# Optimization experiments

Hardware: AMD Instinct MI355X
Metric: run time of the kernel (lower is better)

## Reference

```python
import jax, jax.numpy as jnp
import numpy as np

M = 16
C = 7 * M          # 112, stage-8 channels
CLS = 20
TOPK = 3
NQ = 20000         # current-frame active sites at stage 8
NS = 8192          # support-frame active sites at stage 8
SCALE = 128.0      # voxel coordinate range at this depth


def setup_inputs() -> dict:
    key = jax.random.key(0)
    ks = jax.random.split(key, 9)
    coords_q = jax.random.uniform(ks[0], (NQ, 3), jnp.float32) * SCALE
    coords_s = jax.random.uniform(ks[1], (NS, 3), jnp.float32) * SCALE
    x7 = jax.random.normal(ks[2], (NQ, C), jnp.float32)
    feat_s7 = jax.random.normal(ks[3], (NS, C), jnp.float32)
    feat_s = jax.random.normal(ks[4], (NS, C), jnp.float32)
    w_attn = jax.random.normal(ks[5], (C,), jnp.float32) * 0.1
    W1 = jax.random.normal(ks[6], (2 * C, C), jnp.float32) * (1.0 / np.sqrt(2 * C))
    gamma = jnp.ones((C,), jnp.float32)
    beta = jnp.zeros((C,), jnp.float32)
    W2 = jax.random.normal(ks[7], (C, C), jnp.float32) * (1.0 / np.sqrt(C))
    W_cls = jax.random.normal(ks[8], (C, CLS), jnp.float32) * (1.0 / np.sqrt(C))
    b_cls = jnp.zeros((CLS,), jnp.float32)
    return dict(coords_q=coords_q, coords_s=coords_s, x7=x7, feat_s7=feat_s7,
                feat_s=feat_s, w_attn=w_attn, W1=W1, gamma=gamma, beta=beta,
                W2=W2, W_cls=W_cls, b_cls=b_cls)


def reference(coords_q, coords_s, x7, feat_s7, feat_s, w_attn, W1, gamma, beta, W2, W_cls, b_cls):
    # GlobalMeanAttentionPooling: attention-weighted mean over support sites -> global vector [C]
    a = jax.nn.softmax(feat_s7 @ w_attn)          # [NS]
    g = a @ feat_s7                                # [C]
    # GlobalMaskLayer: channel-wise sigmoid gating of current-frame features
    feat_q = x7 * jax.nn.sigmoid(g)                # [NQ, C]
    # DistMatchLayer_v4: top-3 nearest support voxels per query, softmax(-d2) weighting
    q2 = jnp.sum(coords_q * coords_q, -1, keepdims=True)   # [NQ, 1]
    s2 = jnp.sum(coords_s * coords_s, -1)                  # [NS]
    d2 = q2 + s2[None, :] - 2.0 * (coords_q @ coords_s.T)  # [NQ, NS]
    negd, idx = jax.lax.top_k(-d2, TOPK)                   # [NQ, K]
    w = jax.nn.softmax(negd, axis=-1)                      # [NQ, K]
    matched = jnp.einsum('nk,nkc->nc', w, feat_s[idx])     # [NQ, C]
    # tune_sub: 1x1 subconv (14m->7m) -> BN(eval affine) + ReLU -> 1x1 subconv (7m->7m)
    h = jnp.concatenate([feat_q, matched], -1) @ W1        # [NQ, C]
    h = jax.nn.relu(h * gamma + beta) @ W2                 # [NQ, C]
    # final classifier linear
    return h @ W_cls + b_cls                               # [NQ, CLS]
```

## Files before the change

kernel.cpp:

```cpp
#include <hip/hip_runtime.h>

#define NQv 20000
#define NSv 8192
#define Cv  112
#define CLSv 20
#define INFF 3.4e38f
#define JINF 0x7fffffff

#define GC 16
#define NCELL 4096
#define CELLH 8.0f
#define INVH 0.125f

#define POOLB 32
#define PT 1024
#define PNW (POOLB * PT / 64)

#define MQ 16
#define MB (NQv / MQ)
#define MT 256
#define WS_START 3616
#define WS_PTS4  5668
#define WS_W1TH  38440
#define WS_W1TL  50984
#define WS_W2TH  63528
#define WS_W2TL  70696
#define WS_WCT   77864
#define WS_GATE  80104

typedef __attribute__((ext_vector_type(8))) short bf16x8;
typedef __attribute__((ext_vector_type(4))) float f32x4;
typedef unsigned short us;
typedef unsigned long long u64;

__device__ __forceinline__ float bf2f(us u) {
    union { unsigned int i; float f; } v; v.i = ((unsigned int)u) << 16; return v.f;
}
__device__ __forceinline__ us f2bf(float f) {
    union { float f; unsigned int i; } v; v.f = f;
    unsigned int r = v.i + 0x7fffu + ((v.i >> 16) & 1u);
    return (us)(r >> 16);
}
__device__ __forceinline__ void split(float v, us& h, us& l) {
    h = f2bf(v); l = f2bf(v - bf2f(h));
}

__device__ __forceinline__ u64 mkkey(float e, int j) {
    union { float f; unsigned int i; } v; v.f = e;
    unsigned int ue = v.i ^ ((unsigned int)((int)v.i >> 31) | 0x80000000u);
    return ((u64)ue << 32) | (unsigned int)j;
}
__device__ __forceinline__ float keyval(u64 k) {
    unsigned int ue = (unsigned int)(k >> 32);
    unsigned int u = ue ^ ((unsigned int)((int)(~ue) >> 31) | 0x80000000u);
    union { unsigned int i; float f; } v; v.i = u; return v.f;
}
__device__ __forceinline__ u64 umin64(u64 a, u64 b) { return a < b ? a : b; }
__device__ __forceinline__ u64 umax64(u64 a, u64 b) { return a > b ? a : b; }

__global__ __launch_bounds__(PT) void k_prep(const float* __restrict__ cs,
                                             const float* __restrict__ fs7,
                                             const float* __restrict__ wat,
                                             const float* __restrict__ W1,
                                             const float* __restrict__ W2,
                                             const float* __restrict__ Wc,
                                             float* __restrict__ ws) {
    int b = blockIdx.x, tid = threadIdx.x;

    if (b == POOLB + 1) {
        us* w1h = (us*)(ws + WS_W1TH);
        us* w1l = (us*)(ws + WS_W1TL);
        for (int idx = tid; idx < Cv * 224; idx += PT) {
            int c = idx / 224, k = idx - c * 224;
            us h, l; split(W1[k * Cv + c], h, l);
            w1h[c * 224 + k] = h; w1l[c * 224 + k] = l;
        }
        return;
    }
    if (b == POOLB + 2) {
        us* w2h = (us*)(ws + WS_W2TH);
        us* w2l = (us*)(ws + WS_W2TL);
        for (int idx = tid; idx < Cv * 128; idx += PT) {
            int c = idx >> 7, k = idx & 127;
            float v = (k < Cv) ? W2[k * Cv + c] : 0.f;
            us h, l; split(v, h, l);
            w2h[c * 128 + k] = h; w2l[c * 128 + k] = l;
        }
        float* wct = ws + WS_WCT;
        for (int idx = tid; idx < CLSv * Cv; idx += PT) {
            int cls = idx / Cv, k = idx - cls * Cv;
            wct[cls * Cv + k] = Wc[k * CLSv + cls];
        }
        return;
    }
    if (b == POOLB) {
        __shared__ int cnt[NCELL];
        __shared__ int wsum[PT / 64];
        us* startg = (us*)(ws + WS_START);
        float4* pts4 = (float4*)(ws + WS_PTS4);
        int lane = tid & 63, wv = tid >> 6;
        for (int i = tid; i < NCELL; i += PT) cnt[i] = 0;
        __syncthreads();
        float xx[8], yy[8], zz[8]; int cid[8]; int pp[8];
        #pragma unroll
        for (int k = 0; k < NSv / PT; ++k) {
            int p = k * PT + tid;
            pp[k] = p;
            xx[k] = cs[3 * p]; yy[k] = cs[3 * p + 1]; zz[k] = cs[3 * p + 2];
            int cx = (int)(xx[k] * INVH), cy = (int)(yy[k] * INVH), cz = (int)(zz[k] * INVH);
            cx = cx > 15 ? 15 : cx; cy = cy > 15 ? 15 : cy; cz = cz > 15 ? 15 : cz;
            cid[k] = (cz * GC + cy) * GC + cx;
            atomicAdd(&cnt[cid[k]], 1);
        }
        __syncthreads();
        int base = tid * 4;
        int c0 = cnt[base], c1 = cnt[base + 1], c2 = cnt[base + 2], c3 = cnt[base + 3];
        int local = c0 + c1 + c2 + c3;
        int inc = local;
        #pragma unroll
        for (int off = 1; off < 64; off <<= 1) {
            int v = __shfl_up(inc, off, 64);
            if (lane >= off) inc += v;
        }
        if (lane == 63) wsum[wv] = inc;
        __syncthreads();
        if (tid < PT / 64) {
            int v = wsum[tid];
            #pragma unroll
            for (int off = 1; off < 16; off <<= 1) {
                int o = __shfl_up(v, off, 64);
                if (tid >= off) v += o;
            }
            wsum[tid] = v;
        }
        __syncthreads();
        int wbase = (wv == 0) ? 0 : wsum[wv - 1];
        int run = wbase + inc - local;
        startg[base] = (us)run;     cnt[base] = run;     run += c0;
        startg[base + 1] = (us)run; cnt[base + 1] = run; run += c1;
        startg[base + 2] = (us)run; cnt[base + 2] = run; run += c2;
        startg[base + 3] = (us)run; cnt[base + 3] = run;
        if (tid == 0) startg[NCELL] = (us)NSv;
        __syncthreads();
        #pragma unroll
        for (int k = 0; k < NSv / PT; ++k) {
            int slot = atomicAdd(&cnt[cid[k]], 1);
            pts4[slot] = make_float4(-2.f * xx[k], -2.f * yy[k], -2.f * zz[k], (float)pp[k]);
        }
        return;
    }

    __shared__ float red[PT / 64][Cv + 1];
    int gtid = b * PT + tid;
    int wid = gtid >> 6, lw = tid >> 6, lane = gtid & 63, l2 = lane * 2;
    float2 wa = make_float2(0.f, 0.f);
    if (lane < 56) wa = *(const float2*)(wat + l2);
    float gx = 0.f, gy = 0.f, z = 0.f;
    for (int g = 0; g < 2; ++g) {
        float2 f[8]; float part[8];
        #pragma unroll
        for (int u = 0; u < 8; ++u) {
            int i = wid + (g * 8 + u) * PNW;
            f[u] = (lane < 56) ? *(const float2*)(fs7 + i * Cv + l2) : make_float2(0.f, 0.f);
            part[u] = f[u].x * wa.x + f[u].y * wa.y;
        }
        #pragma unroll
        for (int off = 32; off; off >>= 1)
            #pragma unroll
            for (int u = 0; u < 8; ++u) part[u] += __shfl_xor(part[u], off, 64);
        #pragma unroll
        for (int u = 0; u < 8; ++u) {
            float p = __expf(part[u]);
            gx = fmaf(p, f[u].x, gx); gy = fmaf(p, f[u].y, gy); z += p;
        }
    }
    if (lane < 56) { red[lw][l2] = gx; red[lw][l2 + 1] = gy; }
    if (lane == 0) red[lw][Cv] = z;
    __syncthreads();
    if (tid < Cv + 1) {
        float s = 0.f;
        #pragma unroll
        for (int i = 0; i < PT / 64; ++i) s += red[i][tid];
        ws[tid * POOLB + b] = s;
    }
}

__global__ __launch_bounds__(128) void k_gate(float* __restrict__ ws) {
    int tid = threadIdx.x;
    if (tid < Cv) {
        float st = 0.f, zt = 0.f;
        const float* pr = ws + tid * POOLB;
        const float* zr = ws + Cv * POOLB;
        #pragma unroll
        for (int b = 0; b < POOLB; ++b) { st += pr[b]; zt += zr[b]; }
        ws[WS_GATE + tid] = 1.0f / (1.0f + __expf(-(st / zt)));
    }
}

__device__ __forceinline__ void scan_run(const float4* __restrict__ pts4,
                                         int a, int b, float qx, float qy, float qz,
                                         float& E0, float& E1, float& E2,
                                         int& J0, int& J1, int& J2) {
    for (int k = a; k < b; ++k) {
        float4 P = pts4[k];
        float x = -0.5f * P.x, y = -0.5f * P.y, z = -0.5f * P.z;
        float s2 = fmaf(x, x, fmaf(y, y, z * z));
        float e = fmaf(qx, P.x, fmaf(qy, P.y, fmaf(qz, P.z, s2)));
        int j = (int)P.w;
        bool lt2 = (e < E2) || (e == E2 && j < J2);
        if (lt2) {
            bool lt1 = (e < E1) || (e == E1 && j < J1);
            bool lt0 = (e < E0) || (e == E0 && j < J0);
            E2 = lt1 ? E1 : e;              J2 = lt1 ? J1 : j;
            E1 = lt0 ? E0 : (lt1 ? e : E1); J1 = lt0 ? J0 : (lt1 ? j : J1);
            if (lt0) { E0 = e; J0 = j; }
        }
    }
}

__global__ __launch_bounds__(MT, 6) void k_fused(
        const float* __restrict__ cq,
        const float* __restrict__ x7, const float* __restrict__ fs,
        const float* __restrict__ gma, const float* __restrict__ bta,
        const float* __restrict__ bc, const float* __restrict__ ws,
        float* __restrict__ out) {
    __shared__ __align__(16) us vb[2 * MQ * 232];
    __shared__ __align__(16) us hbh[MQ * 136];
    __shared__ __align__(16) us hbl[MQ * 136];

    us* vbh = vb;
    us* vbl = vb + MQ * 232;
    float* h2f = (float*)vb;

    const us* __restrict__ startg = (const us*)(ws + WS_START);
    const float4* __restrict__ pts4 = (const float4*)(ws + WS_PTS4);

    int tid = threadIdx.x;
    int q0 = blockIdx.x * MQ;
    int sub = tid & 15;
    int qq  = tid >> 4;
    int q   = q0 + qq;

    float4 px[4], g4[4];
    if (sub < 7) {
        const float4* xr = (const float4*)(x7 + q * Cv + sub * 16);
        px[0] = xr[0]; px[1] = xr[1]; px[2] = xr[2]; px[3] = xr[3];
        const float4* gr = (const float4*)(ws + WS_GATE + sub * 16);
        g4[0] = gr[0]; g4[1] = gr[1]; g4[2] = gr[2]; g4[3] = gr[3];
    }
    {
        int zq = tid >> 4, kk = Cv + (tid & 15);
        hbh[zq * 136 + kk] = 0; hbl[zq * 136 + kk] = 0;
    }

    u64 K0 = ~0ull, K1 = ~0ull, K2 = ~0ull;
    {
        float qx = cq[3 * q], qy = cq[3 * q + 1], qz = cq[3 * q + 2];
        float q2 = fmaf(qx, qx, fmaf(qy, qy, qz * qz));
        int cx = (int)(qx * INVH), cy = (int)(qy * INVH), cz = (int)(qz * INVH);
        cx = cx > 15 ? 15 : cx; cy = cy > 15 ? 15 : cy; cz = cz > 15 ? 15 : cz;
        float E0 = INFF, E1 = INFF, E2 = INFF;
        int   J0 = JINF, J1 = JINF, J2 = JINF;

        #pragma unroll
        for (int c = sub; c < 27; c += 16) {
            int dz = c / 9 - 1, dy = (c / 3) % 3 - 1, dx = c % 3 - 1;
            int xc = cx + dx, yc = cy + dy, zc = cz + dz;
            if ((unsigned)xc < 16u && (unsigned)yc < 16u && (unsigned)zc < 16u) {
                int ccell = (zc * GC + yc) * GC + xc;
                scan_run(pts4, startg[ccell], startg[ccell + 1], qx, qy, qz,
                         E0, E1, E2, J0, J1, J2);
            }
        }

        bool done = false;
        for (int s = 2; ; ++s) {
            if (!done) {
                K0 = mkkey(E0, J0); K1 = mkkey(E1, J1); K2 = mkkey(E2, J2);
                #pragma unroll
                for (int off = 1; off < 16; off <<= 1) {
                    u64 b0 = __shfl_xor(K0, off, 64);
                    u64 b1 = __shfl_xor(K1, off, 64);
                    u64 b2 = __shfl_xor(K2, off, 64);
                    u64 xx = umax64(K0, b0), yy = umin64(K1, b1);
                    u64 zz = umax64(K1, b1), uu = umin64(K2, b2);
                    K0 = umin64(K0, b0);
                    u64 n1 = umin64(xx, yy);
                    K2 = umin64(umin64(umax64(xx, yy), zz), uu);
                    K1 = n1;
                }
            }
            if (s > 15) break;
            if (!done) {
                int r = s - 1;
                int xl = cx - r > 0 ? cx - r : 0, xh = cx + r < 15 ? cx + r : 15;
                int yl = cy - r > 0 ? cy - r : 0, yh = cy + r < 15 ? cy + r : 15;
                int zl = cz - r > 0 ? cz - r : 0, zh = cz + r < 15 ? cz + r : 15;
                float fx = INFF, fy = INFF, fz = INFF;
                if (xl > 0)  fx = qx - xl * CELLH;
                if (xh < 15) fx = fminf(fx, (xh + 1) * CELLH - qx);
                if (yl > 0)  fy = qy - yl * CELLH;
                if (yh < 15) fy = fminf(fy, (yh + 1) * CELLH - qy);
                if (zl > 0)  fz = qz - zl * CELLH;
                if (zh < 15) fz = fminf(fz, (zh + 1) * CELLH - qz);
                float dmin = fminf(fx, fminf(fy, fz));
                float t2 = keyval(K2);
                if (dmin * dmin > t2 + q2 + 0.5f) {
                    done = true;
                } else if (s == 2) {
                    for (int idx = sub; idx < 125; idx += 16) {
                        int dz = idx / 25 - 2;
                        int rem = idx - (dz + 2) * 25;
                        int dy = rem / 5 - 2;
                        int dx = rem - (dy + 2) * 5 - 2;
                        int ax = dx < 0 ? -dx : dx, ay = dy < 0 ? -dy : dy, az = dz < 0 ? -dz : dz;
                        if (ax != 2 && ay != 2 && az != 2) continue;
                        int xc = cx + dx, yc = cy + dy, zc = cz + dz;
                        if ((unsigned)xc > 15u || (unsigned)yc > 15u || (unsigned)zc > 15u) continue;
                        int ccell = (zc * GC + yc) * GC + xc;
                        scan_run(pts4, startg[ccell], startg[ccell + 1], qx, qy, qz,
                                 E0, E1, E2, J0, J1, J2);
                    }
                } else {
                    int side = 2 * s + 1, s2n = side * side, tot = s2n * side;
                    for (int idx = sub; idx < tot; idx += 16) {
                        int dz = idx / s2n - s;
                        int rem = idx - (dz + s) * s2n;
                        int dy = rem / side - s;
                        int dx = rem - (dy + s) * side - s;
                        int ax = dx < 0 ? -dx : dx, ay = dy < 0 ? -dy : dy, az = dz < 0 ? -dz : dz;
                        if (ax != s && ay != s && az != s) continue;
                        int xc = cx + dx, yc = cy + dy, zc = cz + dz;
                        if ((unsigned)xc > 15u || (unsigned)yc > 15u || (unsigned)zc > 15u) continue;
                        int ccell = (zc * GC + yc) * GC + xc;
                        scan_run(pts4, startg[ccell], startg[ccell + 1], qx, qy, qz,
                                 E0, E1, E2, J0, J1, J2);
                    }
                }
            }
            if (__all(done)) break;
        }
    }

    {
        unsigned int A0 = (unsigned int)K0;
        unsigned int A1 = (unsigned int)K1;
        unsigned int A2 = (unsigned int)K2;
        if (A0 >= NSv) A0 = 0;
        if (A1 >= NSv) A1 = 0;
        if (A2 >= NSv) A2 = 0;
        if (sub < 7) {
            int k0 = sub * 16;
            float vals[16];
            #pragma unroll
            for (int i = 0; i < 4; ++i) {
                float4 v = px[i], g = g4[i];
                vals[i * 4]     = v.x * g.x;
                vals[i * 4 + 1] = v.y * g.y;
                vals[i * 4 + 2] = v.z * g.z;
                vals[i * 4 + 3] = v.w * g.w;
            }
            #pragma unroll
            for (int i = 0; i < 16; ++i) {
                us h, l; split(vals[i], h, l);
                vbh[qq * 232 + k0 + i] = h;
                vbl[qq * 232 + k0 + i] = l;
            }
        } else if (sub < 14) {
            float e0 = keyval(K0), e1 = keyval(K1), e2 = keyval(K2);
            float w1v = __expf(e0 - e1);
            float w2v = __expf(e0 - e2);
            float iw  = 1.0f / (1.0f + w1v + w2v);
            float w0 = iw, w1 = w1v * iw, w2 = w2v * iw;
            int kk = (sub - 7) * 16;
            const float4* r0 = (const float4*)(fs + A0 * Cv + kk);
            const float4* r1 = (const float4*)(fs + A1 * Cv + kk);
            const float4* r2 = (const float4*)(fs + A2 * Cv + kk);
            float vals[16];
            #pragma unroll
            for (int i = 0; i < 4; ++i) {
                float4 a = r0[i], b = r1[i], c = r2[i];
                vals[i * 4]     = w0 * a.x + w1 * b.x + w2 * c.x;
                vals[i * 4 + 1] = w0 * a.y + w1 * b.y + w2 * c.y;
                vals[i * 4 + 2] = w0 * a.z + w1 * b.z + w2 * c.z;
                vals[i * 4 + 3] = w0 * a.w + w1 * b.w + w2 * c.w;
            }
            int k0 = Cv + kk;
            #pragma unroll
            for (int i = 0; i < 16; ++i) {
                us h, l; split(vals[i], h, l);
                vbh[qq * 232 + k0 + i] = h;
                vbl[qq * 232 + k0 + i] = l;
            }
        }
    }
    __syncthreads();

    int w = tid >> 6, lane = tid & 63, quad = lane >> 4, l16 = lane & 15;
    bool two = (w < 3);
    int cc0 = w * 16 + l16;
    int cc1 = two ? (w + 4) * 16 + l16 : cc0;

    {
        f32x4 acc0 = {0.f, 0.f, 0.f, 0.f};
        f32x4 acc1 = {0.f, 0.f, 0.f, 0.f};
        const us* w1h0 = (const us*)(ws + WS_W1TH) + cc0 * 224;
        const us* w1l0 = (const us*)(ws + WS_W1TL) + cc0 * 224;
        const us* w1h1 = (const us*)(ws + WS_W1TH) + cc1 * 224;
        const us* w1l1 = (const us*)(ws + WS_W1TL) + cc1 * 224;
        #pragma unroll
        for (int ks = 0; ks < 7; ++ks) {
            int ko = ks * 32 + quad * 8;
            bf16x8 ah = *(const bf16x8*)(vbh + l16 * 232 + ko);
            bf16x8 al = *(const bf16x8*)(vbl + l16 * 232 + ko);
            bf16x8 bh0 = *(const bf16x8*)(w1h0 + ko);
            bf16x8 bl0 = *(const bf16x8*)(w1l0 + ko);
            acc0 = __builtin_amdgcn_mfma_f32_16x16x32_bf16(ah, bh0, acc0, 0, 0, 0);
            acc0 = __builtin_amdgcn_mfma_f32_16x16x32_bf16(al, bh0, acc0, 0, 0, 0);
            acc0 = __builtin_amdgcn_mfma_f32_16x16x32_bf16(ah, bl0, acc0, 0, 0, 0);
            if (two) {
                bf16x8 bh1 = *(const bf16x8*)(w1h1 + ko);
                bf16x8 bl1 = *(const bf16x8*)(w1l1 + ko);
                acc1 = __builtin_amdgcn_mfma_f32_16x16x32_bf16(ah, bh1, acc1, 0, 0, 0);
                acc1 = __builtin_amdgcn_mfma_f32_16x16x32_bf16(al, bh1, acc1, 0, 0, 0);
                acc1 = __builtin_amdgcn_mfma_f32_16x16x32_bf16(ah, bl1, acc1, 0, 0, 0);
            }
        }
        float g0 = gma[cc0], b0 = bta[cc0];
        float g1 = two ? gma[cc1] : 0.f, b1 = two ? bta[cc1] : 0.f;
        #pragma unroll
        for (int r = 0; r < 4; ++r) {
            int dq = quad * 4 + r;
            float h = fmaf(acc0[r], g0, b0); h = h > 0.f ? h : 0.f;
            us hh, ll; split(h, hh, ll);
            hbh[dq * 136 + cc0] = hh; hbl[dq * 136 + cc0] = ll;
            if (two) {
                float h2 = fmaf(acc1[r], g1, b1); h2 = h2 > 0.f ? h2 : 0.f;
                split(h2, hh, ll);
                hbh[dq * 136 + cc1] = hh; hbl[dq * 136 + cc1] = ll;
            }
        }
    }
    __syncthreads();

    {
        f32x4 acc0 = {0.f, 0.f, 0.f, 0.f};
        f32x4 acc1 = {0.f, 0.f, 0.f, 0.f};
        const us* w2h0 = (const us*)(ws + WS_W2TH) + cc0 * 128;
        const us* w2l0 = (const us*)(ws + WS_W2TL) + cc0 * 128;
        const us* w2h1 = (const us*)(ws + WS_W2TH) + cc1 * 128;
        const us* w2l1 = (const us*)(ws + WS_W2TL) + cc1 * 128;
        #pragma unroll
        for (int ks = 0; ks < 4; ++ks) {
            int ko = ks * 32 + quad * 8;
            bf16x8 ah = *(const bf16x8*)(hbh + l16 * 136 + ko);
            bf16x8 al = *(const bf16x8*)(hbl + l16 * 136 + ko);
            bf16x8 bh0 = *(const bf16x8*)(w2h0 + ko);
            bf16x8 bl0 = *(const bf16x8*)(w2l0 + ko);
            acc0 = __builtin_amdgcn_mfma_f32_16x16x32_bf16(ah, bh0, acc0, 0, 0, 0);
            acc0 = __builtin_amdgcn_mfma_f32_16x16x32_bf16(al, bh0, acc0, 0, 0, 0);
            acc0 = __builtin_amdgcn_mfma_f32_16x16x32_bf16(ah, bl0, acc0, 0, 0, 0);
            if (two) {
                bf16x8 bh1 = *(const bf16x8*)(w2h1 + ko);
                bf16x8 bl1 = *(const bf16x8*)(w2l1 + ko);
                acc1 = __builtin_amdgcn_mfma_f32_16x16x32_bf16(ah, bh1, acc1, 0, 0, 0);
                acc1 = __builtin_amdgcn_mfma_f32_16x16x32_bf16(al, bh1, acc1, 0, 0, 0);
                acc1 = __builtin_amdgcn_mfma_f32_16x16x32_bf16(ah, bl1, acc1, 0, 0, 0);
            }
        }
        #pragma unroll
        for (int r = 0; r < 4; ++r) {
            int dq = quad * 4 + r;
            h2f[dq * 116 + cc0] = acc0[r];
            if (two) h2f[dq * 116 + cc1] = acc1[r];
        }
    }
    __syncthreads();

    for (int it = tid; it < MQ * CLSv; it += MT) {
        int cls = it % CLSv, oq = it / CLSv;
        const float4* wr = (const float4*)(ws + WS_WCT + cls * Cv);
        const float4* hr = (const float4*)(h2f + oq * 116);
        float a = bc[cls];
        #pragma unroll 7
        for (int i = 0; i < 28; ++i) {
            float4 h = hr[i], v = wr[i];
            a = fmaf(h.x, v.x, fmaf(h.y, v.y, fmaf(h.z, v.z, fmaf(h.w, v.w, a))));
        }
        out[(q0 + oq) * CLSv + cls] = a;
    }
}

extern "C" void kernel_launch(void* const* d_in, const int* in_sizes, int n_in,
                              void* d_out, int out_size, void* d_ws, size_t ws_size,
                              hipStream_t stream) {
    const float* cq  = (const float*)d_in[0];
    const float* cs  = (const float*)d_in[1];
    const float* x7  = (const float*)d_in[2];
    const float* fs7 = (const float*)d_in[3];
    const float* fs  = (const float*)d_in[4];
    const float* wat = (const float*)d_in[5];
    const float* W1  = (const float*)d_in[6];
    const float* gma = (const float*)d_in[7];
    const float* bta = (const float*)d_in[8];
    const float* W2  = (const float*)d_in[9];
    const float* Wc  = (const float*)d_in[10];
    const float* bc  = (const float*)d_in[11];
    float* ws  = (float*)d_ws;
    float* out = (float*)d_out;

    k_prep<<<POOLB + 3, PT, 0, stream>>>(cs, fs7, wat, W1, W2, Wc, ws);
    k_gate<<<1, 128, 0, stream>>>(ws);
    k_fused<<<MB, MT, 0, stream>>>(cq, x7, fs, gma, bta, bc, ws, out);
}
```

Measured before the change: 149.8 us.

## Double query tile, fold gate kernel into fused kernel, unroll neighbor scan

Raises the per-block query tile from 16 to 32 with 512 threads, so each of 7 waves owns one 16-column output slice and reuses its weight fragments across two query row-tiles. This is meant to halve the weight loads per query in the MFMA stages. The separate gate kernel launch is removed and every block now recomputes the sigmoid gate into shared memory, which saves a launch but adds a redundant reduction per block. The grid scan loop is unrolled by two to overlap point loads, and one of the eight waves sits idle during the matmul stages.

```diff
diff --git a/kernel.cpp b/kernel.cpp
--- a/kernel.cpp
+++ b/kernel.cpp
@@ -16,9 +16,9 @@
 #define PT 1024
 #define PNW (POOLB * PT / 64)
 
-#define MQ 16
+#define MQ 32
 #define MB (NQv / MQ)
-#define MT 256
+#define MT 512
 #define WS_START 3616
 #define WS_PTS4  5668
 #define WS_W1TH  38440
@@ -26,7 +26,6 @@
 #define WS_W2TH  63528
 #define WS_W2TL  70696
 #define WS_WCT   77864
-#define WS_GATE  80104
 
 typedef __attribute__((ext_vector_type(8))) short bf16x8;
 typedef __attribute__((ext_vector_type(4))) float f32x4;
@@ -185,15 +184,20 @@
     }
 }
 
-__global__ __launch_bounds__(128) void k_gate(float* __restrict__ ws) {
-    int tid = threadIdx.x;
-    if (tid < Cv) {
-        float st = 0.f, zt = 0.f;
-        const float* pr = ws + tid * POOLB;
-        const float* zr = ws + Cv * POOLB;
-        #pragma unroll
-        for (int b = 0; b < POOLB; ++b) { st += pr[b]; zt += zr[b]; }
-        ws[WS_GATE + tid] = 1.0f / (1.0f + __expf(-(st / zt)));
+__device__ __forceinline__ void ins_pt(float4 P, float qx, float qy, float qz,
+                                       float& E0, float& E1, float& E2,
+                                       int& J0, int& J1, int& J2) {
+    float x = -0.5f * P.x, y = -0.5f * P.y, z = -0.5f * P.z;
+    float s2 = fmaf(x, x, fmaf(y, y, z * z));
+    float e = fmaf(qx, P.x, fmaf(qy, P.y, fmaf(qz, P.z, s2)));
+    int j = (int)P.w;
+    bool lt2 = (e < E2) || (e == E2 && j < J2);
+    if (lt2) {
+        bool lt1 = (e < E1) || (e == E1 && j < J1);
+        bool lt0 = (e < E0) || (e == E0 && j < J0);
+        E2 = lt1 ? E1 : e;              J2 = lt1 ? J1 : j;
+        E1 = lt0 ? E0 : (lt1 ? e : E1); J1 = lt0 ? J0 : (lt1 ? j : J1);
+        if (lt0) { E0 = e; J0 = j; }
     }
 }
 
@@ -201,20 +205,16 @@
                                          int a, int b, float qx, float qy, float qz,
                                          float& E0, float& E1, float& E2,
                                          int& J0, int& J1, int& J2) {
-    for (int k = a; k < b; ++k) {
-        float4 P = pts4[k];
-        float x = -0.5f * P.x, y = -0.5f * P.y, z = -0.5f * P.z;
-        float s2 = fmaf(x, x, fmaf(y, y, z * z));
-        float e = fmaf(qx, P.x, fmaf(qy, P.y, fmaf(qz, P.z, s2)));
-        int j = (int)P.w;
-        bool lt2 = (e < E2) || (e == E2 && j < J2);
-        if (lt2) {
-            bool lt1 = (e < E1) || (e == E1 && j < J1);
-            bool lt0 = (e < E0) || (e == E0 && j < J0);
-            E2 = lt1 ? E1 : e;              J2 = lt1 ? J1 : j;
-            E1 = lt0 ? E0 : (lt1 ? e : E1); J1 = lt0 ? J0 : (lt1 ? j : J1);
-            if (lt0) { E0 = e; J0 = j; }
-        }
+    int k = a;
+    for (; k + 2 <= b; k += 2) {
+        float4 P0 = pts4[k];
+        float4 P1 = pts4[k + 1];
+        ins_pt(P0, qx, qy, qz, E0, E1, E2, J0, J1, J2);
+        ins_pt(P1, qx, qy, qz, E0, E1, E2, J0, J1, J2);
+    }
+    if (k < b) {
+        float4 P0 = pts4[k];
+        ins_pt(P0, qx, qy, qz, E0, E1, E2, J0, J1, J2);
     }
 }
 
@@ -227,6 +227,7 @@
     __shared__ __align__(16) us vb[2 * MQ * 232];
     __shared__ __align__(16) us hbh[MQ * 136];
     __shared__ __align__(16) us hbl[MQ * 136];
+    __shared__ float gate[Cv];
 
     us* vbh = vb;
     us* vbl = vb + MQ * 232;
@@ -241,17 +242,25 @@
     int qq  = tid >> 4;
     int q   = q0 + qq;
 
-    float4 px[4], g4[4];
+    float4 px[4];
     if (sub < 7) {
         const float4* xr = (const float4*)(x7 + q * Cv + sub * 16);
         px[0] = xr[0]; px[1] = xr[1]; px[2] = xr[2]; px[3] = xr[3];
-        const float4* gr = (const float4*)(ws + WS_GATE + sub * 16);
-        g4[0] = gr[0]; g4[1] = gr[1]; g4[2] = gr[2]; g4[3] = gr[3];
+    }
+
+    if (tid < Cv) {
+        float st = 0.f, zt = 0.f;
+        const float* pr = ws + tid * POOLB;
+        const float* zr = ws + Cv * POOLB;
+        #pragma unroll
+        for (int b = 0; b < POOLB; ++b) { st += pr[b]; zt += zr[b]; }
+        gate[tid] = 1.0f / (1.0f + __expf(-(st / zt)));
     }
     {
         int zq = tid >> 4, kk = Cv + (tid & 15);
         hbh[zq * 136 + kk] = 0; hbl[zq * 136 + kk] = 0;
     }
+    __syncthreads();
 
     u64 K0 = ~0ull, K1 = ~0ull, K2 = ~0ull;
     {
@@ -351,6 +360,7 @@
         if (A2 >= NSv) A2 = 0;
         if (sub < 7) {
             int k0 = sub * 16;
+            const float4* g4 = (const float4*)(gate + k0);
             float vals[16];
             #pragma unroll
             for (int i = 0; i < 4; ++i) {
@@ -397,82 +407,69 @@
     __syncthreads();
 
     int w = tid >> 6, lane = tid & 63, quad = lane >> 4, l16 = lane & 15;
-    bool two = (w < 3);
-    int cc0 = w * 16 + l16;
-    int cc1 = two ? (w + 4) * 16 + l16 : cc0;
-
-    {
+    int cc = (w < 7 ? w : 0) * 16 + l16;
+
+    if (w < 7) {
         f32x4 acc0 = {0.f, 0.f, 0.f, 0.f};
         f32x4 acc1 = {0.f, 0.f, 0.f, 0.f};
-        const us* w1h0 = (const us*)(ws + WS_W1TH) + cc0 * 224;
-        const us* w1l0 = (const us*)(ws + WS_W1TL) + cc0 * 224;
-        const us* w1h1 = (const us*)(ws + WS_W1TH) + cc1 * 224;
-        const us* w1l1 = (const us*)(ws + WS_W1TL) + cc1 * 224;
+        const us* w1h = (const us*)(ws + WS_W1TH) + cc * 224;
+        const us* w1l = (const us*)(ws + WS_W1TL) + cc * 224;
         #pragma unroll
         for (int ks = 0; ks < 7; ++ks) {
             int ko = ks * 32 + quad * 8;
-            bf16x8 ah = *(const bf16x8*)(vbh + l16 * 232 + ko);
-            bf16x8 al = *(const bf16x8*)(vbl + l16 * 232 + ko);
-            bf16x8 bh0 = *(const bf16x8*)(w1h0 + ko);
-            bf16x8 bl0 = *(const bf16x8*)(w1l0 + ko);
-            acc0 = __builtin_amdgcn_mfma_f32_16x16x32_bf16(ah, bh0, acc0, 0, 0, 0);
-            acc0 = __builtin_amdgcn_mfma_f32_16x16x32_bf16(al, bh0, acc0, 0, 0, 0);
-            acc0 = __builtin_amdgcn_mfma_f32_16x16x32_bf16(ah, bl0, acc0, 0, 0, 0);
-            if (two) {
-                bf16x8 bh1 = *(const bf16x8*)(w1h1 + ko);
-                bf16x8 bl1 = *(const bf16x8*)(w1l1 + ko);
-                acc1 = __builtin_amdgcn_mfma_f32_16x16x32_bf16(ah, bh1, acc1, 0, 0, 0);
-                acc1 = __builtin_amdgcn_mfma_f32_16x16x32_bf16(al, bh1, acc1, 0, 0, 0);
-                acc1 = __builtin_amdgcn_mfma_f32_16x16x32_bf16(ah, bl1, acc1, 0, 0, 0);
-            }
-        }
-        float g0 = gma[cc0], b0 = bta[cc0];
-        float g1 = two ? gma[cc1] : 0.f, b1 = two ? bta[cc1] : 0.f;
+            bf16x8 bh  = *(const bf16x8*)(w1h + ko);
+            bf16x8 bl  = *(const bf16x8*)(w1l + ko);
+            bf16x8 a0h = *(const bf16x8*)(vbh + l16 * 232 + ko);
+            bf16x8 a0l = *(const bf16x8*)(vbl + l16 * 232 + ko);
+            bf16x8 a1h = *(const bf16x8*)(vbh + (l16 + 16) * 232 + ko);
+            bf16x8 a1l = *(const bf16x8*)(vbl + (l16 + 16) * 232 + ko);
+            acc0 = __builtin_amdgcn_mfma_f32_16x16x32_bf16(a0h, bh, acc0, 0, 0, 0);
+            acc0 = __builtin_amdgcn_mfma_f32_16x16x32_bf16(a0l, bh, acc0, 0, 0, 0);
+            acc0 = __builtin_amdgcn_mfma_f32_16x16x32_bf16(a0h, bl, acc0, 0, 0, 0);
+            acc1 = __builtin_amdgcn_mfma_f32_16x16x32_bf16(a1h, bh, acc1, 0, 0, 0);
+            acc1 = __builtin_amdgcn_mfma_f32_16x16x32_bf16(a1l, bh, acc1, 0, 0, 0);
+            acc1 = __builtin_amdgcn_mfma_f32_16x16x32_bf16(a1h, bl, acc1, 0, 0, 0);
+        }
+        float g = gma[cc], bb = bta[cc];
         #pragma unroll
         for (int r = 0; r < 4; ++r) {
             int dq = quad * 4 + r;
-            float h = fmaf(acc0[r], g0, b0); h = h > 0.f ? h : 0.f;
+            float h = fmaf(acc0[r], g, bb); h = h > 0.f ? h : 0.f;
             us hh, ll; split(h, hh, ll);
-            hbh[dq * 136 + cc0] = hh; hbl[dq * 136 + cc0] = ll;
-            if (two) {
-                float h2 = fmaf(acc1[r], g1, b1); h2 = h2 > 0.f ? h2 : 0.f;
-                split(h2, hh, ll);
-                hbh[dq * 136 + cc1] = hh; hbl[dq * 136 + cc1] = ll;
-            }
+            hbh[dq * 136 + cc] = hh; hbl[dq * 136 + cc] = ll;
+            float h2 = fmaf(acc1[r], g, bb); h2 = h2 > 0.f ? h2 : 0.f;
+            split(h2, hh, ll);
+            hbh[(dq + 16) * 136 + cc] = hh; hbl[(dq + 16) * 136 + cc] = ll;
         }
     }
     __syncthreads();
 
-    {
+    if (w < 7) {
         f32x4 acc0 = {0.f, 0.f, 0.f, 0.f};
         f32x4 acc1 = {0.f, 0.f, 0.f, 0.f};
-        const us* w2h0 = (const us*)(ws + WS_W2TH) + cc0 * 128;
-        const us* w2l0 = (const us*)(ws + WS_W2TL) + cc0 * 128;
-        const us* w2h1 = (const us*)(ws + WS_W2TH) + cc1 * 128;
-        const us* w2l1 = (const us*)(ws + WS_W2TL) + cc1 * 128;
+        const us* w2h = (const us*)(ws + WS_W2TH) + cc * 128;
+        const us* w2l = (const us*)(ws + WS_W2TL) + cc * 128;
         #pragma unroll
         for (int ks = 0; ks < 4; ++ks) {
             int ko = ks * 32 + quad * 8;
-            bf16x8 ah = *(const bf16x8*)(hbh + l16 * 136 + ko);
-            bf16x8 al = *(const bf16x8*)(hbl + l16 * 136 + ko);
-            bf16x8 bh0 = *(const bf16x8*)(w2h0 + ko);
-            bf16x8 bl0 = *(const bf16x8*)(w2l0 + ko);
-            acc0 = __builtin_amdgcn_mfma_f32_16x16x32_bf16(ah, bh0, acc0, 0, 0, 0);
-            acc0 = __builtin_amdgcn_mfma_f32_16x16x32_bf16(al, bh0, acc0, 0, 0, 0);
-            acc0 = __builtin_amdgcn_mfma_f32_16x16x32_bf16(ah, bl0, acc0, 0, 0, 0);
-            if (two) {
-                bf16x8 bh1 = *(const bf16x8*)(w2h1 + ko);
-                bf16x8 bl1 = *(const bf16x8*)(w2l1 + ko);
-                acc1 = __builtin_amdgcn_mfma_f32_16x16x32_bf16(ah, bh1, acc1, 0, 0, 0);
-                acc1 = __builtin_amdgcn_mfma_f32_16x16x32_bf16(al, bh1, acc1, 0, 0, 0);
-                acc1 = __builtin_amdgcn_mfma_f32_16x16x32_bf16(ah, bl1, acc1, 0, 0, 0);
-            }
+            bf16x8 bh  = *(const bf16x8*)(w2h + ko);
+            bf16x8 bl  = *(const bf16x8*)(w2l + ko);
+            bf16x8 a0h = *(const bf16x8*)(hbh + l16 * 136 + ko);
+            bf16x8 a0l = *(const bf16x8*)(hbl + l16 * 136 + ko);
+            bf16x8 a1h = *(const bf16x8*)(hbh + (l16 + 16) * 136 + ko);
+            bf16x8 a1l = *(const bf16x8*)(hbl + (l16 + 16) * 136 + ko);
+            acc0 = __builtin_amdgcn_mfma_f32_16x16x32_bf16(a0h, bh, acc0, 0, 0, 0);
+            acc0 = __builtin_amdgcn_mfma_f32_16x16x32_bf16(a0l, bh, acc0, 0, 0, 0);
+            acc0 = __builtin_amdgcn_mfma_f32_16x16x32_bf16(a0h, bl, acc0, 0, 0, 0);
+            acc1 = __builtin_amdgcn_mfma_f32_16x16x32_bf16(a1h, bh, acc1, 0, 0, 0);
+            acc1 = __builtin_amdgcn_mfma_f32_16x16x32_bf16(a1l, bh, acc1, 0, 0, 0);
+            acc1 = __builtin_amdgcn_mfma_f32_16x16x32_bf16(a1h, bl, acc1, 0, 0, 0);
         }
         #pragma unroll
         for (int r = 0; r < 4; ++r) {
             int dq = quad * 4 + r;
-            h2f[dq * 116 + cc0] = acc0[r];
-            if (two) h2f[dq * 116 + cc1] = acc1[r];
+            h2f[dq * 116 + cc] = acc0[r];
+            h2f[(dq + 16) * 116 + cc] = acc1[r];
         }
     }
     __syncthreads();
@@ -510,6 +507,5 @@
     float* out = (float*)d_out;
 
     k_prep<<<POOLB + 3, PT, 0, stream>>>(cs, fs7, wat, W1, W2, Wc, ws);
-    k_gate<<<1, 128, 0, stream>>>(ws);
     k_fused<<<MB, MT, 0, stream>>>(cq, x7, fs, gma, bta, bc, ws, out);
 }
```

Measured after the change: 142.0 us (median of 2 runs). 5.2% less time.
